# Performance work log

Measured on AMD Instinct MI355X. Metric: run time of the kernel, lower is better.

## Reference

```python
import jax, jax.numpy as jnp
import numpy as np

EPS = 1e-08
LAMBDA_SIM = 1.0
LAMBDA_SPARSITY = 0.001
B, D, K = 8192, 4096, 64


def setup_inputs() -> dict:
    key = jax.random.key(0)
    k1, k2, k3, k4, k5 = jax.random.split(key, 5)
    labels = jax.random.randint(k1, (B,), 0, K)
    hard_class_probs = jax.nn.one_hot(labels, K, dtype=jnp.float32)  # [B,K] hard one-hot
    return {
        "hard_class_probs": hard_class_probs,
        "masked_activations_1b": jax.random.normal(k2, (B, D), dtype=jnp.float32),
        "masked_activations_8b": jax.random.normal(k3, (B, D), dtype=jnp.float32),
        "mask_1b": jax.random.uniform(k4, (B, D), dtype=jnp.float32),
        "mask_8b": jax.random.uniform(k5, (B, D), dtype=jnp.float32),
    }


def _classwise_pairwise_cossim(acts, hard_class_probs):
    # F.normalize(p=2, dim=-1, eps=EPS): x / max(||x||, eps)
    norms = jnp.sqrt(jnp.sum(acts * acts, axis=-1, keepdims=True))
    norm_acts = acts / jnp.maximum(norms, EPS)                      # [B,D]
    S = norm_acts @ norm_acts.T                                      # [B,B] gram of unit vectors
    diag = jnp.sum(norm_acts * norm_acts, axis=-1)                   # [B] (== diag(S))
    M = (hard_class_probs > 0.5).astype(acts.dtype)                  # [B,K] hard membership
    n = jnp.sum(M, axis=0)                                           # [K] class counts
    SM = S @ M                                                       # [B,K]
    mSm = jnp.sum(M * SM, axis=0)                                    # [K] sum_{i,j in class} S_ij
    sum_diag = M.T @ diag                                            # [K]
    pair_sum = 0.5 * (mSm - sum_diag)                                # sum over i<j pairs
    n_pairs = 0.5 * n * (n - 1.0)
    valid = n >= 2.0
    per_class_mean = jnp.where(valid, pair_sum / jnp.maximum(n_pairs, 1.0), 0.0)
    n_valid = jnp.sum(valid.astype(acts.dtype))
    return jnp.where(n_valid > 0, jnp.sum(per_class_mean) / jnp.maximum(n_valid, 1.0), 0.0)


def _binary_entropy(p):
    p = jnp.clip(p, EPS, 1.0 - EPS)
    return jnp.mean(-(p * jnp.log(p) + (1.0 - p) * jnp.log(1.0 - p)))


def _combined_loss(hard_class_probs, masked_activations, mask):
    sim_loss = -_classwise_pairwise_cossim(masked_activations, hard_class_probs)
    sparsity_loss = _binary_entropy(mask)
    total = LAMBDA_SIM * sim_loss + LAMBDA_SPARSITY * sparsity_loss
    return total, sim_loss, sparsity_loss


def reference(hard_class_probs, masked_activations_1b, masked_activations_8b, mask_1b, mask_8b):
    loss_1b, sim_1b, sp_1b = _combined_loss(hard_class_probs, masked_activations_1b, mask_1b)
    loss_8b, sim_8b, sp_8b = _combined_loss(hard_class_probs, masked_activations_8b, mask_8b)
    total_loss = loss_1b + loss_8b
    return (total_loss, sim_1b, sim_8b, sp_1b, sp_8b)
```

## Files before the change

kernel.cpp:

```cpp
#include <hip/hip_runtime.h>
#include <math.h>

#define B_ 8192
#define D_ 4096
#define K_ 64
#define EPSF 1e-8f
#define LN2F 0.69314718056f
#define ENT_GRID 2048
#define SPLITS 16

typedef float f32x4 __attribute__((ext_vector_type(4)));


__global__ void k_init(int* __restrict__ z) {
  if (threadIdx.x < 192) z[threadIdx.x] = 0;
}

__global__ void k_labels(const float* __restrict__ probs, int* __restrict__ labels,
                         int* __restrict__ counts, int* __restrict__ rowlist) {
  int row = blockIdx.x * 4 + (threadIdx.x >> 6);
  int lane = threadIdx.x & 63;
  float p = probs[(size_t)row * K_ + lane];
  unsigned long long m = __ballot(p > 0.5f);
  if (lane == 0) {
    int k = __ffsll(m) - 1;
    if (k >= 0) {
      labels[row] = k;
      int pos = atomicAdd(&counts[k], 1);
      rowlist[k * B_ + pos] = row;
    }
  }
}

__global__ __launch_bounds__(256) void k_classnorm(
    const float* __restrict__ a1, const float* __restrict__ a8,
    const int* __restrict__ counts, const int* __restrict__ rowlist,
    float* __restrict__ Cpart1, float* __restrict__ Cpart8, float* __restrict__ sd1,
    float* __restrict__ sd8) {
  __shared__ float lred[2][4];
  int bid = blockIdx.x;
  const int NBLK = K_ * SPLITS;
  const float* a = (bid < NBLK) ? a1 : a8;
  float* Cpart = (bid < NBLK) ? Cpart1 : Cpart8;
  float* sd = (bid < NBLK) ? sd1 : sd8;
  bid = (bid < NBLK) ? bid : bid - NBLK;
  int k = bid & 63;
  int split = bid >> 6;
  int wave = threadIdx.x >> 6;
  int lane = threadIdx.x & 63;
  int cnt = counts[k];
  int beg = (cnt * split) / SPLITS;
  int end = (cnt * (split + 1)) / SPLITS;
  const int* rl = rowlist + k * B_;

  f32x4 acc0 = 0.f, acc1 = 0.f, acc2 = 0.f, acc3 = 0.f;
  int par = 0;
  for (int r = beg; r < end; ++r, par ^= 1) {
    int row = rl[r];
    const f32x4* rp = (const f32x4*)(a + (size_t)row * D_) + (wave * 256 + lane);
    f32x4 v0 = rp[0];
    f32x4 v1 = rp[64];
    f32x4 v2 = rp[128];
    f32x4 v3 = rp[192];
    float s = v0.x * v0.x + v0.y * v0.y + v0.z * v0.z + v0.w * v0.w;
    s += v1.x * v1.x + v1.y * v1.y + v1.z * v1.z + v1.w * v1.w;
    s += v2.x * v2.x + v2.y * v2.y + v2.z * v2.z + v2.w * v2.w;
    s += v3.x * v3.x + v3.y * v3.y + v3.z * v3.z + v3.w * v3.w;
#pragma unroll
    for (int o = 32; o > 0; o >>= 1) s += __shfl_xor(s, o);
    if (lane == 0) lred[par][wave] = s;
    __syncthreads();
    float stot = lred[par][0] + lred[par][1] + lred[par][2] + lred[par][3];
    float w = 1.0f / fmaxf(sqrtf(stot), EPSF);
    acc0 += w * v0;
    acc1 += w * v1;
    acc2 += w * v2;
    acc3 += w * v3;
    if (threadIdx.x == 0) atomicAdd(&sd[k], stot * w * w);
  }

  float* cp = Cpart + ((size_t)split * K_ + k) * D_ + wave * 1024;
  *(f32x4*)(cp + 4 * lane) = acc0;
  *(f32x4*)(cp + 4 * (64 + lane)) = acc1;
  *(f32x4*)(cp + 4 * (128 + lane)) = acc2;
  *(f32x4*)(cp + 4 * (192 + lane)) = acc3;
}

__global__ __launch_bounds__(256) void k_msm(const float* __restrict__ Cpart1,
                                             const float* __restrict__ Cpart8,
                                             float* __restrict__ msp1,
                                             float* __restrict__ msp8) {
  __shared__ float lds[4];
  int b = blockIdx.x;
  const float* Cpart = (b < 256) ? Cpart1 : Cpart8;
  float* msp = (b < 256) ? msp1 : msp8;
  b &= 255;
  int k = b >> 2;
  int q = b & 3;
  int t = threadIdx.x;
  int col = q * 1024 + 4 * t;
  f32x4 c = 0.f;
#pragma unroll
  for (int s = 0; s < SPLITS; ++s)
    c += *(const f32x4*)(Cpart + ((size_t)s * K_ + k) * D_ + col);
  float sq = c.x * c.x + c.y * c.y + c.z * c.z + c.w * c.w;
#pragma unroll
  for (int o = 32; o > 0; o >>= 1) sq += __shfl_down(sq, o);
  if ((t & 63) == 0) lds[t >> 6] = sq;
  __syncthreads();
  if (t == 0) msp[blockIdx.x & 255] = lds[0] + lds[1] + lds[2] + lds[3];
}

__device__ __forceinline__ float ent1(float p) {
  p = fminf(fmaxf(p, EPSF), 1.0f - EPSF);
  float q = 1.0f - p;
  float lp = __builtin_amdgcn_logf(p);
  float lq = __builtin_amdgcn_logf(fmaxf(q, 1e-38f));
  return -(p * lp + q * lq);
}

__device__ __forceinline__ float ent4(f32x4 v) {
  return ent1(v.x) + ent1(v.y) + ent1(v.z) + ent1(v.w);
}

__global__ __launch_bounds__(256) void k_entropy(const f32x4* __restrict__ m1,
                                                 const f32x4* __restrict__ m8,
                                                 double* __restrict__ entpart) {
  __shared__ float lds[8];
  const int CHUNK = (B_ * D_ / 4) / ENT_GRID;
  int base = blockIdx.x * CHUNK;
  int t = threadIdx.x;
  float s1 = 0.f, s8 = 0.f;
#pragma unroll
  for (int o = 0; o < 4; ++o) {
    f32x4 a[4], b[4];
#pragma unroll
    for (int j = 0; j < 4; ++j) {
      int idx = base + t + (o * 4 + j) * 256;
      a[j] = m1[idx];
      b[j] = m8[idx];
    }
#pragma unroll
    for (int j = 0; j < 4; ++j) {
      s1 += ent4(a[j]);
      s8 += ent4(b[j]);
    }
  }
#pragma unroll
  for (int o = 32; o > 0; o >>= 1) {
    s1 += __shfl_down(s1, o);
    s8 += __shfl_down(s8, o);
  }
  int wid = t >> 6;
  if ((t & 63) == 0) { lds[wid] = s1; lds[4 + wid] = s8; }
  __syncthreads();
  if (t == 0) {
    float t1 = lds[0] + lds[1] + lds[2] + lds[3];
    float t8 = lds[4] + lds[5] + lds[6] + lds[7];
    entpart[blockIdx.x]            = (double)(t1 * LN2F);
    entpart[ENT_GRID + blockIdx.x] = (double)(t8 * LN2F);
  }
}

__global__ void k_final(const double* __restrict__ entpart, const int* __restrict__ counts,
                        const float* __restrict__ sd1, const float* __restrict__ sd8,
                        const float* __restrict__ msp1, const float* __restrict__ msp8,
                        float* __restrict__ out) {
  __shared__ double dl[8];
  int t = threadIdx.x;
  double e1 = 0.0, e8 = 0.0;
  for (int i = t; i < ENT_GRID; i += 256) {
    e1 += entpart[i];
    e8 += entpart[ENT_GRID + i];
  }
#pragma unroll
  for (int o = 32; o > 0; o >>= 1) {
    e1 += __shfl_down(e1, o);
    e8 += __shfl_down(e8, o);
  }
  int wid = t >> 6;
  if ((t & 63) == 0) { dl[wid] = e1; dl[4 + wid] = e8; }
  __syncthreads();
  float pcm1 = 0.f, pcm8 = 0.f, valid = 0.f;
  if (t < K_) {
    float mSm1 = msp1[t * 4] + msp1[t * 4 + 1] + msp1[t * 4 + 2] + msp1[t * 4 + 3];
    float mSm8 = msp8[t * 4] + msp8[t * 4 + 1] + msp8[t * 4 + 2] + msp8[t * 4 + 3];
    float n = (float)counts[t];
    bool v = (n >= 2.0f);
    float np = fmaxf(0.5f * n * (n - 1.0f), 1.0f);
    valid = v ? 1.0f : 0.f;
    pcm1 = v ? 0.5f * (mSm1 - sd1[t]) / np : 0.f;
    pcm8 = v ? 0.5f * (mSm8 - sd8[t]) / np : 0.f;
  }
#pragma unroll
  for (int o = 32; o > 0; o >>= 1) {
    pcm1 += __shfl_down(pcm1, o);
    pcm8 += __shfl_down(pcm8, o);
    valid += __shfl_down(valid, o);
  }
  if (t == 0) {
    double etot1 = dl[0] + dl[1] + dl[2] + dl[3];
    double etot8 = dl[4] + dl[5] + dl[6] + dl[7];
    float sp1 = (float)(etot1 / (double)((long long)B_ * D_));
    float sp8 = (float)(etot8 / (double)((long long)B_ * D_));
    float cs1 = (valid > 0.f) ? pcm1 / fmaxf(valid, 1.0f) : 0.f;
    float cs8 = (valid > 0.f) ? pcm8 / fmaxf(valid, 1.0f) : 0.f;
    float sim1 = -cs1, sim8 = -cs8;
    out[0] = sim1 + sim8 + 0.001f * (sp1 + sp8);
    out[1] = sim1;
    out[2] = sim8;
    out[3] = sp1;
    out[4] = sp8;
  }
}


extern "C" void kernel_launch(void* const* d_in, const int* in_sizes, int n_in,
                              void* d_out, int out_size, void* d_ws, size_t ws_size,
                              hipStream_t stream) {
  const float* probs = (const float*)d_in[0];
  const float* a1 = (const float*)d_in[1];
  const float* a8 = (const float*)d_in[2];
  const float* m1 = (const float*)d_in[3];
  const float* m8 = (const float*)d_in[4];
  float* out = (float*)d_out;
  char* ws = (char*)d_ws;

  double* entpart = (double*)(ws + 0);
  int* labels = (int*)(ws + 32768);
  int* counts = (int*)(ws + 65536);
  float* sd1 = (float*)(ws + 65792);
  float* sd8 = (float*)(ws + 66048);
  float* msp1 = (float*)(ws + 66304);
  float* msp8 = (float*)(ws + 67328);
  int* rowlist = (int*)(ws + 69632);
  float* Cpart1 = (float*)(ws + 2166784);
  float* Cpart8 = (float*)(ws + 18944000);

  k_init<<<1, 256, 0, stream>>>(counts);
  k_labels<<<B_ / 4, 256, 0, stream>>>(probs, labels, counts, rowlist);
  k_classnorm<<<2 * K_ * SPLITS, 256, 0, stream>>>(a1, a8, counts, rowlist, Cpart1, Cpart8,
                                                   sd1, sd8);
  k_entropy<<<ENT_GRID, 256, 0, stream>>>((const f32x4*)m1, (const f32x4*)m8, entpart);
  k_msm<<<512, 256, 0, stream>>>(Cpart1, Cpart8, msp1, msp8);
  k_final<<<1, 256, 0, stream>>>(entpart, counts, sd1, sd8, msp1, msp8, out);
}
```

Before: 193.1 us.

## Fuse class-norm accumulation and entropy into one interleaved kernel

Merges the class-wise normalized-sum kernel and the binary-entropy kernel into a single launch, with odd blocks computing entropy and even blocks accumulating class sums, so the two bandwidth-bound phases overlap instead of running back to back. Per-row atomicAdd on the diagonal sum is replaced by a per-block register accumulation followed by one atomic. The unused labels write is dropped and entropy chunks are resized to 1024 per tensor. Interleaving changes block scheduling and load balance between the two kinds of work.

```diff
diff --git a/kernel.cpp b/kernel.cpp
--- a/kernel.cpp
+++ b/kernel.cpp
@@ -6,8 +6,8 @@
 #define K_ 64
 #define EPSF 1e-8f
 #define LN2F 0.69314718056f
-#define ENT_GRID 2048
 #define SPLITS 16
+#define ECHUNKS 1024
 
 typedef float f32x4 __attribute__((ext_vector_type(4)));
 
@@ -16,8 +16,8 @@
   if (threadIdx.x < 192) z[threadIdx.x] = 0;
 }
 
-__global__ void k_labels(const float* __restrict__ probs, int* __restrict__ labels,
-                         int* __restrict__ counts, int* __restrict__ rowlist) {
+__global__ void k_labels(const float* __restrict__ probs, int* __restrict__ counts,
+                         int* __restrict__ rowlist) {
   int row = blockIdx.x * 4 + (threadIdx.x >> 6);
   int lane = threadIdx.x & 63;
   float p = probs[(size_t)row * K_ + lane];
@@ -25,65 +25,99 @@
   if (lane == 0) {
     int k = __ffsll(m) - 1;
     if (k >= 0) {
-      labels[row] = k;
       int pos = atomicAdd(&counts[k], 1);
       rowlist[k * B_ + pos] = row;
     }
   }
 }
 
-__global__ __launch_bounds__(256) void k_classnorm(
+__device__ __forceinline__ float ent1(float p) {
+  p = fminf(fmaxf(p, EPSF), 1.0f - EPSF);
+  float q = 1.0f - p;
+  float lp = __builtin_amdgcn_logf(p);
+  float lq = __builtin_amdgcn_logf(fmaxf(q, 1e-38f));
+  return -(p * lp + q * lq);
+}
+
+__device__ __forceinline__ float ent4(f32x4 v) {
+  return ent1(v.x) + ent1(v.y) + ent1(v.z) + ent1(v.w);
+}
+
+__global__ __launch_bounds__(256) void k_fused(
     const float* __restrict__ a1, const float* __restrict__ a8,
+    const f32x4* __restrict__ m1, const f32x4* __restrict__ m8,
     const int* __restrict__ counts, const int* __restrict__ rowlist,
     float* __restrict__ Cpart1, float* __restrict__ Cpart8, float* __restrict__ sd1,
-    float* __restrict__ sd8) {
-  __shared__ float lred[2][4];
-  int bid = blockIdx.x;
-  const int NBLK = K_ * SPLITS;
-  const float* a = (bid < NBLK) ? a1 : a8;
-  float* Cpart = (bid < NBLK) ? Cpart1 : Cpart8;
-  float* sd = (bid < NBLK) ? sd1 : sd8;
-  bid = (bid < NBLK) ? bid : bid - NBLK;
-  int k = bid & 63;
-  int split = bid >> 6;
-  int wave = threadIdx.x >> 6;
-  int lane = threadIdx.x & 63;
-  int cnt = counts[k];
-  int beg = (cnt * split) / SPLITS;
-  int end = (cnt * (split + 1)) / SPLITS;
-  const int* rl = rowlist + k * B_;
-
-  f32x4 acc0 = 0.f, acc1 = 0.f, acc2 = 0.f, acc3 = 0.f;
-  int par = 0;
-  for (int r = beg; r < end; ++r, par ^= 1) {
-    int row = rl[r];
-    const f32x4* rp = (const f32x4*)(a + (size_t)row * D_) + (wave * 256 + lane);
-    f32x4 v0 = rp[0];
-    f32x4 v1 = rp[64];
-    f32x4 v2 = rp[128];
-    f32x4 v3 = rp[192];
-    float s = v0.x * v0.x + v0.y * v0.y + v0.z * v0.z + v0.w * v0.w;
-    s += v1.x * v1.x + v1.y * v1.y + v1.z * v1.z + v1.w * v1.w;
-    s += v2.x * v2.x + v2.y * v2.y + v2.z * v2.z + v2.w * v2.w;
-    s += v3.x * v3.x + v3.y * v3.y + v3.z * v3.z + v3.w * v3.w;
-#pragma unroll
-    for (int o = 32; o > 0; o >>= 1) s += __shfl_xor(s, o);
-    if (lane == 0) lred[par][wave] = s;
+    float* __restrict__ sd8, double* __restrict__ entpart) {
+  __shared__ float sh[8];
+  int t = threadIdx.x;
+  if (blockIdx.x & 1) {
+    int blk = blockIdx.x >> 1;
+    const f32x4* base = ((blk < ECHUNKS) ? m1 : m8) + (size_t)(blk & (ECHUNKS - 1)) * 8192;
+    double* ep = entpart + ((blk < ECHUNKS) ? 0 : ECHUNKS);
+    float s = 0.f;
+#pragma unroll
+    for (int o = 0; o < 4; ++o) {
+      f32x4 v[8];
+#pragma unroll
+      for (int j = 0; j < 8; ++j) v[j] = base[t + (o * 8 + j) * 256];
+#pragma unroll
+      for (int j = 0; j < 8; ++j) s += ent4(v[j]);
+    }
+#pragma unroll
+    for (int o = 32; o > 0; o >>= 1) s += __shfl_down(s, o);
+    if ((t & 63) == 0) sh[t >> 6] = s;
     __syncthreads();
-    float stot = lred[par][0] + lred[par][1] + lred[par][2] + lred[par][3];
-    float w = 1.0f / fmaxf(sqrtf(stot), EPSF);
-    acc0 += w * v0;
-    acc1 += w * v1;
-    acc2 += w * v2;
-    acc3 += w * v3;
-    if (threadIdx.x == 0) atomicAdd(&sd[k], stot * w * w);
-  }
-
-  float* cp = Cpart + ((size_t)split * K_ + k) * D_ + wave * 1024;
-  *(f32x4*)(cp + 4 * lane) = acc0;
-  *(f32x4*)(cp + 4 * (64 + lane)) = acc1;
-  *(f32x4*)(cp + 4 * (128 + lane)) = acc2;
-  *(f32x4*)(cp + 4 * (192 + lane)) = acc3;
+    if (t == 0) ep[blk & (ECHUNKS - 1)] = (double)((sh[0] + sh[1] + sh[2] + sh[3]) * LN2F);
+  } else {
+    int bid2 = blockIdx.x >> 1;
+    const float* a = (bid2 < 1024) ? a1 : a8;
+    float* Cpart = (bid2 < 1024) ? Cpart1 : Cpart8;
+    float* sd = (bid2 < 1024) ? sd1 : sd8;
+    int b2 = bid2 & 1023;
+    int k = b2 & 63;
+    int split = b2 >> 6;
+    int wave = t >> 6;
+    int lane = t & 63;
+    int cnt = counts[k];
+    int beg = (cnt * split) / SPLITS;
+    int end = (cnt * (split + 1)) / SPLITS;
+    const int* rl = rowlist + k * B_;
+
+    f32x4 acc0 = 0.f, acc1 = 0.f, acc2 = 0.f, acc3 = 0.f;
+    float sdacc = 0.f;
+    int par = 0;
+    for (int r = beg; r < end; ++r, par ^= 1) {
+      int row = rl[r];
+      const f32x4* rp = (const f32x4*)(a + (size_t)row * D_) + (wave * 256 + lane);
+      f32x4 v0 = rp[0];
+      f32x4 v1 = rp[64];
+      f32x4 v2 = rp[128];
+      f32x4 v3 = rp[192];
+      float s = v0.x * v0.x + v0.y * v0.y + v0.z * v0.z + v0.w * v0.w;
+      s += v1.x * v1.x + v1.y * v1.y + v1.z * v1.z + v1.w * v1.w;
+      s += v2.x * v2.x + v2.y * v2.y + v2.z * v2.z + v2.w * v2.w;
+      s += v3.x * v3.x + v3.y * v3.y + v3.z * v3.z + v3.w * v3.w;
+#pragma unroll
+      for (int o = 32; o > 0; o >>= 1) s += __shfl_xor(s, o);
+      if (lane == 0) sh[par * 4 + wave] = s;
+      __syncthreads();
+      float stot = sh[par * 4] + sh[par * 4 + 1] + sh[par * 4 + 2] + sh[par * 4 + 3];
+      float w = 1.0f / fmaxf(sqrtf(stot), EPSF);
+      acc0 += w * v0;
+      acc1 += w * v1;
+      acc2 += w * v2;
+      acc3 += w * v3;
+      sdacc += stot * w * w;
+    }
+
+    float* cp = Cpart + ((size_t)split * K_ + k) * D_ + wave * 1024;
+    *(f32x4*)(cp + 4 * lane) = acc0;
+    *(f32x4*)(cp + 4 * (64 + lane)) = acc1;
+    *(f32x4*)(cp + 4 * (128 + lane)) = acc2;
+    *(f32x4*)(cp + 4 * (192 + lane)) = acc3;
+    if (t == 0 && sdacc != 0.f) atomicAdd(&sd[k], sdacc);
+  }
 }
 
 __global__ __launch_bounds__(256) void k_msm(const float* __restrict__ Cpart1,
@@ -111,57 +145,6 @@
   if (t == 0) msp[blockIdx.x & 255] = lds[0] + lds[1] + lds[2] + lds[3];
 }
 
-__device__ __forceinline__ float ent1(float p) {
-  p = fminf(fmaxf(p, EPSF), 1.0f - EPSF);
-  float q = 1.0f - p;
-  float lp = __builtin_amdgcn_logf(p);
-  float lq = __builtin_amdgcn_logf(fmaxf(q, 1e-38f));
-  return -(p * lp + q * lq);
-}
-
-__device__ __forceinline__ float ent4(f32x4 v) {
-  return ent1(v.x) + ent1(v.y) + ent1(v.z) + ent1(v.w);
-}
-
-__global__ __launch_bounds__(256) void k_entropy(const f32x4* __restrict__ m1,
-                                                 const f32x4* __restrict__ m8,
-                                                 double* __restrict__ entpart) {
-  __shared__ float lds[8];
-  const int CHUNK = (B_ * D_ / 4) / ENT_GRID;
-  int base = blockIdx.x * CHUNK;
-  int t = threadIdx.x;
-  float s1 = 0.f, s8 = 0.f;
-#pragma unroll
-  for (int o = 0; o < 4; ++o) {
-    f32x4 a[4], b[4];
-#pragma unroll
-    for (int j = 0; j < 4; ++j) {
-      int idx = base + t + (o * 4 + j) * 256;
-      a[j] = m1[idx];
-      b[j] = m8[idx];
-    }
-#pragma unroll
-    for (int j = 0; j < 4; ++j) {
-      s1 += ent4(a[j]);
-      s8 += ent4(b[j]);
-    }
-  }
-#pragma unroll
-  for (int o = 32; o > 0; o >>= 1) {
-    s1 += __shfl_down(s1, o);
-    s8 += __shfl_down(s8, o);
-  }
-  int wid = t >> 6;
-  if ((t & 63) == 0) { lds[wid] = s1; lds[4 + wid] = s8; }
-  __syncthreads();
-  if (t == 0) {
-    float t1 = lds[0] + lds[1] + lds[2] + lds[3];
-    float t8 = lds[4] + lds[5] + lds[6] + lds[7];
-    entpart[blockIdx.x]            = (double)(t1 * LN2F);
-    entpart[ENT_GRID + blockIdx.x] = (double)(t8 * LN2F);
-  }
-}
-
 __global__ void k_final(const double* __restrict__ entpart, const int* __restrict__ counts,
                         const float* __restrict__ sd1, const float* __restrict__ sd8,
                         const float* __restrict__ msp1, const float* __restrict__ msp8,
@@ -169,9 +152,9 @@
   __shared__ double dl[8];
   int t = threadIdx.x;
   double e1 = 0.0, e8 = 0.0;
-  for (int i = t; i < ENT_GRID; i += 256) {
+  for (int i = t; i < ECHUNKS; i += 256) {
     e1 += entpart[i];
-    e8 += entpart[ENT_GRID + i];
+    e8 += entpart[ECHUNKS + i];
   }
 #pragma unroll
   for (int o = 32; o > 0; o >>= 1) {
@@ -227,21 +210,19 @@
   char* ws = (char*)d_ws;
 
   double* entpart = (double*)(ws + 0);
-  int* labels = (int*)(ws + 32768);
-  int* counts = (int*)(ws + 65536);
-  float* sd1 = (float*)(ws + 65792);
-  float* sd8 = (float*)(ws + 66048);
-  float* msp1 = (float*)(ws + 66304);
-  float* msp8 = (float*)(ws + 67328);
-  int* rowlist = (int*)(ws + 69632);
-  float* Cpart1 = (float*)(ws + 2166784);
-  float* Cpart8 = (float*)(ws + 18944000);
+  int* counts = (int*)(ws + 16384);
+  float* sd1 = (float*)(ws + 16640);
+  float* sd8 = (float*)(ws + 16896);
+  float* msp1 = (float*)(ws + 17152);
+  float* msp8 = (float*)(ws + 18176);
+  int* rowlist = (int*)(ws + 32768);
+  float* Cpart1 = (float*)(ws + 2129920);
+  float* Cpart8 = (float*)(ws + 18907136);
 
   k_init<<<1, 256, 0, stream>>>(counts);
-  k_labels<<<B_ / 4, 256, 0, stream>>>(probs, labels, counts, rowlist);
-  k_classnorm<<<2 * K_ * SPLITS, 256, 0, stream>>>(a1, a8, counts, rowlist, Cpart1, Cpart8,
-                                                   sd1, sd8);
-  k_entropy<<<ENT_GRID, 256, 0, stream>>>((const f32x4*)m1, (const f32x4*)m8, entpart);
+  k_labels<<<B_ / 4, 256, 0, stream>>>(probs, counts, rowlist);
+  k_fused<<<4096, 256, 0, stream>>>(a1, a8, (const f32x4*)m1, (const f32x4*)m8, counts,
+                                    rowlist, Cpart1, Cpart8, sd1, sd8, entpart);
   k_msm<<<512, 256, 0, stream>>>(Cpart1, Cpart8, msp1, msp8);
   k_final<<<1, 256, 0, stream>>>(entpart, counts, sd1, sd8, msp1, msp8, out);
 }
```

Measured after the change: 169.6 us, median of 2. 12.1% less time.
